# Kernel optimization log

Measured on AMD Instinct MI355X. Metric: run time of the kernel, lower is better.

Reference implementation:

```python
import jax, jax.numpy as jnp
import numpy as np

K = 8                      # batch_k
NONZERO_CUTOFF = 1.4       # nonzero_loss_cutoff
MARGIN = 1.0               # F.triplet_margin_loss default (module's margin arg is unused)
PD_EPS = 1e-6              # torch pairwise_distance eps


def setup_inputs() -> dict:
    key = jax.random.key(0)
    x = jax.random.normal(key, (4096, 128), dtype=jnp.float32)
    return {"x": x}


def _sample_indices(x, key):
    """Distance-weighted negative sampling; returns (a_idx, p_idx, n_idx), each [n*(K-1)]."""
    n, d = x.shape
    # per-row L2 normalize (eps added to norm, as in original)
    xn = x / (jnp.sqrt(jnp.sum(x * x, axis=1, keepdims=True)) + 1e-5)
    # pairwise euclidean distance; identity added under sqrt exactly as original
    sq = jnp.sum(xn * xn, axis=1, keepdims=True)               # [n,1]
    dist2 = sq + sq.T - 2.0 * (xn @ xn.T)                       # [n,n]
    dist = jnp.sqrt(dist2 + jnp.eye(n, dtype=x.dtype))          # [n,n]
    # distance-weighted sampling log-weights (Wu et al.)
    log_w = (2.0 - d) * jnp.log(dist) - (d - 3) / 2.0 * jnp.log(1.0 - 0.25 * dist * dist)
    w = jnp.exp(log_w - jnp.max(log_w))
    # block mask: same-block pairs excluded
    block = jnp.arange(n) // K                                  # [n]
    mask = (block[:, None] != block[None, :]).astype(x.dtype)
    w = w * mask * (dist < NONZERO_CUTOFF).astype(x.dtype)
    row_sum = jnp.sum(w, axis=1, keepdims=True)
    # rows where weights are degenerate fall back to uniform (original's try/except)
    valid = jnp.isfinite(row_sum) & (row_sum > 0) & jnp.all(jnp.isfinite(w), axis=1, keepdims=True)
    logits = jnp.where(valid, jnp.where(w > 0, jnp.log(w), -jnp.inf), 0.0)   # [n,n]
    # batched categorical sampling via Gumbel-max: K-1 negatives per anchor
    g = jax.random.gumbel(key, (n, K - 1, n), dtype=jnp.float32)
    n_idx = jnp.argmax(logits[:, None, :] + g, axis=-1).reshape(-1)          # [n*(K-1)]
    # anchor/positive pairs: for each i, all other members of its block
    r = jnp.arange(n) % K                                       # position in block
    off = jnp.arange(K - 1)
    p_off = jnp.where(off[None, :] < r[:, None], off[None, :], off[None, :] + 1)
    p_idx = (block[:, None] * K + p_off).reshape(-1)            # [n*(K-1)]
    a_idx = jnp.repeat(jnp.arange(n), K - 1)                    # [n*(K-1)]
    return a_idx, p_idx, n_idx


def reference(x) -> jnp.ndarray:
    key = jax.random.key(42)
    a_idx, p_idx, n_idx = _sample_indices(x, key)
    a, p, ng = x[a_idx], x[p_idx], x[n_idx]
    d_ap = jnp.sqrt(jnp.sum((a - p + PD_EPS) ** 2, axis=1))
    d_an = jnp.sqrt(jnp.sum((a - ng + PD_EPS) ** 2, axis=1))
    return jnp.mean(jnp.maximum(d_ap - d_an + MARGIN, 0.0))
```

## Files before the change

kernel.cpp:

```cpp
#include <hip/hip_runtime.h>
#include <stdint.h>

#define NROWS 4096
#define DIM   128
#define KB    8
#define NS    7
#define TCH   16
#define NPAIR 2048
#define HALF_CNT 58720256u

typedef __bf16 v8bf __attribute__((ext_vector_type(8)));
typedef float  v4f  __attribute__((ext_vector_type(4)));

__device__ __forceinline__ uint32_t rotl32(uint32_t x, int r) {
    return __builtin_amdgcn_alignbit(x, x, 32 - r);
}

__device__ __forceinline__ void threefry2x32(uint32_t c0, uint32_t c1,
                                             uint32_t& o0, uint32_t& o1) {
    const uint32_t ks0 = 0u;
    const uint32_t ks1 = 42u;
    const uint32_t ks2 = 0x1BD11BDAu ^ ks0 ^ ks1;
    uint32_t x0 = c0 + ks0;
    uint32_t x1 = c1 + ks1;
#define TF_R(r) { x0 += x1; x1 = rotl32(x1, r); x1 ^= x0; }
    TF_R(13) TF_R(15) TF_R(26) TF_R(6)
    x0 += ks1; x1 += ks2 + 1u;
    TF_R(17) TF_R(29) TF_R(16) TF_R(24)
    x0 += ks2; x1 += ks0 + 2u;
    TF_R(13) TF_R(15) TF_R(26) TF_R(6)
    x0 += ks0; x1 += ks1 + 3u;
    TF_R(17) TF_R(29) TF_R(16) TF_R(24)
    x0 += ks1; x1 += ks2 + 4u;
    TF_R(13) TF_R(15) TF_R(26) TF_R(6)
    x0 += ks2; x1 += ks0 + 5u;
#undef TF_R
    o0 = x0; o1 = x1;
}

__device__ __forceinline__ float gumbel_of(uint32_t b) {
    float f = __uint_as_float((b >> 9) | 0x3f800000u) - 1.0f;
    float u = f + 1.17549435e-38f;
    float l1 = __log2f(u);
    float inner = -0.69314718055994531f * l1;
    float l2 = __log2f(inner);
    return -0.69314718055994531f * l2;
}

__global__ void knorm(const float* __restrict__ x, __bf16* __restrict__ xb,
                      float* __restrict__ sqv) {
    const int i = blockIdx.x;
    const int t = threadIdx.x;
    float2 v = ((const float2*)(x + (size_t)i * DIM))[t];
    float s = v.x * v.x + v.y * v.y;
#pragma unroll
    for (int m = 32; m > 0; m >>= 1) s += __shfl_xor(s, m, 64);
    float norm = sqrtf(s) + 1e-5f;
    float ox = v.x / norm, oy = v.y / norm;
    union { __bf16 b[2]; uint32_t u; } ph;
    ph.b[0] = (__bf16)ox; ph.b[1] = (__bf16)oy;
    ((uint32_t*)xb)[i * 64 + t] = ph.u;
    float s2 = ox * ox + oy * oy;
#pragma unroll
    for (int m = 32; m > 0; m >>= 1) s2 += __shfl_xor(s2, m, 64);
    if (t == 0) sqv[i] = s2;
}

__global__ __launch_bounds__(256, 4) void kdist(
        const __bf16* __restrict__ xb, const float* __restrict__ sqv,
        int* __restrict__ cnt, unsigned short* __restrict__ t16,
        float2* __restrict__ nwp) {
    const int lane  = threadIdx.x & 63;
    const int chunk = (blockIdx.x << 2) + (threadIdx.x >> 6);
    const int grp   = blockIdx.y;
    const int rlo = lane & 15;
    const int khi = lane >> 4;
    const unsigned int below = (1u << rlo) - 1u;

    const int afr = grp * 8 + (rlo >> 1) + ((rlo & 1) << 11);
    v8bf ah[4];
#pragma unroll
    for (int ks = 0; ks < 4; ++ks)
        ah[ks] = *(const v8bf*)(xb + (size_t)afr * DIM + ks * 32 + khi * 8);

    const int base = grp * 8 + khi * 2;
    float sqA[4];
    sqA[0] = sqv[base];
    sqA[1] = sqv[base + 2048];
    sqA[2] = sqv[base + 1];
    sqA[3] = sqv[base + 2049];

    const int rbA = ((base)     * 16 + chunk) << 8;
    const int rbB = ((base + 1) * 16 + chunk) << 8;
    unsigned int cA = 0, cB = 0;

    const int tcol0 = chunk * 256 + rlo;

    v8bf bhn[4];
    float sqn;
    {
        const size_t boff = (size_t)tcol0 * DIM + khi * 8;
#pragma unroll
        for (int ks = 0; ks < 4; ++ks) bhn[ks] = *(const v8bf*)(xb + boff + ks * 32);
        sqn = sqv[tcol0];
    }

#pragma unroll 1
    for (int cg = 0; cg < 16; ++cg) {
        v8bf bhc[4];
#pragma unroll
        for (int ks = 0; ks < 4; ++ks) bhc[ks] = bhn[ks];
        const float sqB = sqn;
        const int tcol = tcol0 + cg * 16;

        if (cg < 15) {
            const size_t boff = (size_t)(tcol + 16) * DIM + khi * 8;
#pragma unroll
            for (int ks = 0; ks < 4; ++ks) bhn[ks] = *(const v8bf*)(xb + boff + ks * 32);
            sqn = sqv[tcol + 16];
        }

        v4f acc = {0.f, 0.f, 0.f, 0.f};
#pragma unroll
        for (int ks = 0; ks < 4; ++ks)
            acc = __builtin_amdgcn_mfma_f32_16x16x32_bf16(ah[ks], bhc[ks], acc, 0, 0, 0);

        const int tBlk = tcol >> 3;
        const bool bd0 = (tBlk != grp);
        const bool bd1 = (tBlk != grp + 256);

        float nw[4];
        bool  ic[4];
#pragma unroll
        for (int q = 0; q < 4; ++q) {
            float d2  = fmaf(-2.0f, acc[q], sqA[q] + sqB);
            float l1  = __log2f(d2);
            float t2  = fmaf(-0.25f, d2, 1.0f);
            float l2  = __log2f(t2);
            float wiv = exp2f(fmaf(63.0f, l1, 62.5f * l2));
            bool incl = (d2 < 1.96f) && ((q & 1) ? bd1 : bd0);
            ic[q] = incl;
            nw[q] = incl ? -wiv : -INFINITY;
        }

        const bool uA = ic[0] | ic[1];
        const bool uB = ic[2] | ic[3];
        unsigned long long ballA = __ballot(uA);
        unsigned long long ballB = __ballot(uB);
        unsigned int subA = (unsigned int)((ballA >> (khi * 16)) & 0xFFFFull);
        unsigned int subB = (unsigned int)((ballB >> (khi * 16)) & 0xFFFFull);
        if (uA) {
            int slot = rbA + (int)cA + __popc(subA & below);
            t16[slot] = (unsigned short)tcol;
            nwp[slot] = make_float2(nw[0], nw[1]);
        }
        if (uB) {
            int slot = rbB + (int)cB + __popc(subB & below);
            t16[slot] = (unsigned short)tcol;
            nwp[slot] = make_float2(nw[2], nw[3]);
        }
        cA += (unsigned int)__popc(subA);
        cB += (unsigned int)__popc(subB);
    }

    if (rlo == 0) {
        cnt[base * 16 + chunk]       = (int)cA;
        cnt[(base + 1) * 16 + chunk] = (int)cB;
    }
}

__global__ __launch_bounds__(256, 4) void kgum(
        const int* __restrict__ cnt, const unsigned short* __restrict__ t16,
        const float2* __restrict__ nwp, int* __restrict__ nidx) {
    const int p    = blockIdx.x;
    const int wid  = threadIdx.x >> 6;
    const int lane = threadIdx.x & 63;
    const uint32_t pb0 = ((uint32_t)p * 7u) << 12;

    unsigned long long bA[NS], bB[NS];
#pragma unroll
    for (int j = 0; j < NS; ++j) { bA[j] = ~0ull; bB[j] = ~0ull; }

#pragma unroll 1
    for (int c = wid * 4; c < wid * 4 + 4; ++c) {
        const int rid = p * 16 + c;
        const int n  = cnt[rid];
        const int rb = rid << 8;
#pragma unroll 1
        for (int e = lane; e < n; e += 64) {
            const uint32_t t = t16[rb + e];
            const float2 nw  = nwp[rb + e];
#pragma unroll
            for (int j = 0; j < NS; ++j) {
                const uint32_t L = pb0 + ((uint32_t)j << 12) + t;
                uint32_t o0, o1;
                threefry2x32(L, L + HALF_CNT, o0, o1);
                float fA = __uint_as_float((o0 >> 9) | 0x3f800000u) - 1.0f;
                float fB = __uint_as_float((o1 >> 9) | 0x3f800000u) - 1.0f;
                float kA = __log2f(fA + 1.17549435e-38f) * nw.x;
                float kB = __log2f(fB + 1.17549435e-38f) * nw.y;
                unsigned long long pA =
                    ((unsigned long long)__float_as_uint(kA) << 32) | t;
                unsigned long long pB =
                    ((unsigned long long)__float_as_uint(kB) << 32) | t;
                bA[j] = pA < bA[j] ? pA : bA[j];
                bB[j] = pB < bB[j] ? pB : bB[j];
            }
        }
    }

#pragma unroll
    for (int j = 0; j < NS; ++j) {
#pragma unroll
        for (int m = 1; m < 64; m <<= 1) {
            unsigned long long vA = __shfl_xor(bA[j], m, 64);
            unsigned long long vB = __shfl_xor(bB[j], m, 64);
            bA[j] = vA < bA[j] ? vA : bA[j];
            bB[j] = vB < bB[j] ? vB : bB[j];
        }
    }

    __shared__ unsigned long long sA[4][NS], sB[4][NS];
    if (lane == 0) {
#pragma unroll
        for (int j = 0; j < NS; ++j) { sA[wid][j] = bA[j]; sB[wid][j] = bB[j]; }
    }
    __syncthreads();
    if (threadIdx.x < 2 * NS) {
        const int r = threadIdx.x / NS, j = threadIdx.x - r * NS;
        unsigned long long v = r ? sB[0][j] : sA[0][j];
#pragma unroll
        for (int w = 1; w < 4; ++w) {
            unsigned long long v2 = r ? sB[w][j] : sA[w][j];
            v = v2 < v ? v2 : v;
        }
        uint32_t kb = (uint32_t)(v >> 32);
        nidx[(p + r * 2048) * NS + j] = (kb >= 0x7F800000u) ? -1
                                                            : (int)(v & 0xFFFFu);
    }
}

__global__ __launch_bounds__(256, 2) void ksample(
        const __bf16* __restrict__ xb, const float* __restrict__ sqv,
        float* __restrict__ pV, int* __restrict__ pI) {
    const int lane  = threadIdx.x & 63;
    const int chunk = (blockIdx.x << 2) + (threadIdx.x >> 6);
    const int grp   = blockIdx.y;
    const int rlo = lane & 15;
    const int khi = lane >> 4;

    const int afr = grp * 8 + (rlo >> 1) + ((rlo & 1) << 11);
    v8bf ah[4];
#pragma unroll
    for (int ks = 0; ks < 4; ++ks)
        ah[ks] = *(const v8bf*)(xb + (size_t)afr * DIM + ks * 32 + khi * 8);
    const int base = grp * 8 + khi * 2;
    float sqA[4];
    sqA[0] = sqv[base];
    sqA[1] = sqv[base + 2048];
    sqA[2] = sqv[base + 1];
    sqA[3] = sqv[base + 2049];
    const uint32_t P0 = (uint32_t)base;
    const uint32_t P1 = (uint32_t)(base + 1);

    float    bestV[4][NS];
    uint32_t bestP[4];
#pragma unroll
    for (int q = 0; q < 4; ++q) {
        bestP[q] = 0u;
#pragma unroll
        for (int j = 0; j < NS; ++j) bestV[q][j] = INFINITY;
    }
    const int tcol0 = chunk * 256 + rlo;

    v8bf bhn[4];
    float sqn;
    {
        const size_t boff = (size_t)tcol0 * DIM + khi * 8;
#pragma unroll
        for (int ks = 0; ks < 4; ++ks) bhn[ks] = *(const v8bf*)(xb + boff + ks * 32);
        sqn = sqv[tcol0];
    }

#pragma unroll 1
    for (int cg = 0; cg < 16; ++cg) {
        v8bf bhc[4];
#pragma unroll
        for (int ks = 0; ks < 4; ++ks) bhc[ks] = bhn[ks];
        const float sqB = sqn;
        const int tcol = tcol0 + cg * 16;
        if (cg < 15) {
            const size_t boff = (size_t)(tcol + 16) * DIM + khi * 8;
#pragma unroll
            for (int ks = 0; ks < 4; ++ks) bhn[ks] = *(const v8bf*)(xb + boff + ks * 32);
            sqn = sqv[tcol + 16];
        }
        v4f acc = {0.f, 0.f, 0.f, 0.f};
#pragma unroll
        for (int ks = 0; ks < 4; ++ks)
            acc = __builtin_amdgcn_mfma_f32_16x16x32_bf16(ah[ks], bhc[ks], acc, 0, 0, 0);
        const int tBlk = tcol >> 3;
        const bool bd0 = (tBlk != grp);
        const bool bd1 = (tBlk != grp + 256);
        float nw[4];
#pragma unroll
        for (int q = 0; q < 4; ++q) {
            float d2  = fmaf(-2.0f, acc[q], sqA[q] + sqB);
            float l1  = __log2f(d2);
            float t2  = fmaf(-0.25f, d2, 1.0f);
            float l2  = __log2f(t2);
            float wiv = exp2f(fmaf(63.0f, l1, 62.5f * l2));
            bool incl = (d2 < 1.96f) && ((q & 1) ? bd1 : bd0);
            nw[q] = incl ? -wiv : -INFINITY;
        }
        const uint32_t tB = (uint32_t)tcol;
#pragma unroll
        for (int j = 0; j < NS; ++j) {
            uint32_t L0 = ((P0 * 7u + (uint32_t)j) << 12) + tB;
            uint32_t L1 = ((P1 * 7u + (uint32_t)j) << 12) + tB;
            uint32_t o0, o1, o2, o3;
            threefry2x32(L0, L0 + HALF_CNT, o0, o1);
            threefry2x32(L1, L1 + HALF_CNT, o2, o3);
            float vv[4];
            vv[0] = __log2f(__uint_as_float((o0 >> 9) | 0x3f800000u) - 1.0f + 1.17549435e-38f) * nw[0];
            vv[1] = __log2f(__uint_as_float((o1 >> 9) | 0x3f800000u) - 1.0f + 1.17549435e-38f) * nw[1];
            vv[2] = __log2f(__uint_as_float((o2 >> 9) | 0x3f800000u) - 1.0f + 1.17549435e-38f) * nw[2];
            vv[3] = __log2f(__uint_as_float((o3 >> 9) | 0x3f800000u) - 1.0f + 1.17549435e-38f) * nw[3];
            const uint32_t keep = ~(0xFu << (4 * j));
            const uint32_t put  = ((uint32_t)cg) << (4 * j);
#pragma unroll
            for (int q = 0; q < 4; ++q) {
                bool lt = vv[q] < bestV[q][j];
                uint32_t np = (bestP[q] & keep) | put;
                bestV[q][j] = lt ? vv[q] : bestV[q][j];
                bestP[q]    = lt ? np : bestP[q];
            }
        }
    }
#pragma unroll
    for (int q = 0; q < 4; ++q) {
        const int a = base + (q >> 1) + ((q & 1) << 11);
#pragma unroll
        for (int j = 0; j < NS; ++j) {
            float v = bestV[q][j];
            int idx = tcol0 + (int)((bestP[q] >> (4 * j)) & 0xFu) * 16;
#pragma unroll
            for (int m = 1; m < 16; m <<= 1) {
                float v2 = __shfl_xor(v, m, 16);
                int   i2 = __shfl_xor(idx, m, 16);
                if (v2 < v || (v2 == v && i2 < idx)) { v = v2; idx = i2; }
            }
            if (rlo == 0) {
                size_t s = ((size_t)a * NS + j) * TCH + chunk;
                pV[s] = v;
                pI[s] = idx;
            }
        }
    }
}

__global__ void kcombine(const float* __restrict__ pV, const int* __restrict__ pI,
                         int* __restrict__ nidx, int nc) {
    int s = blockIdx.x * 256 + threadIdx.x;
    if (s >= NROWS * NS) return;
    float bv = INFINITY;
    int bi = 0x7FFFFFFF;
    for (int c = 0; c < nc; ++c) {
        float v = pV[(size_t)s * nc + c];
        int idx = pI[(size_t)s * nc + c];
        if (v < bv || (v == bv && idx < bi)) { bv = v; bi = idx; }
    }
    nidx[s] = (bv == INFINITY) ? -1 : bi;
}

__global__ void kfixup(int* __restrict__ nidx) {
    const int i = blockIdx.x;
    if (nidx[(size_t)i * NS] >= 0) return;
    const int lane = threadIdx.x;
    for (int j = 0; j < NS; ++j) {
        float bv = -INFINITY;
        int bi = 0x7FFFFFFF;
        for (int t = lane; t < NROWS; t += 64) {
            uint32_t o0, o1;
            float g;
            if (i < 2048) {
                uint32_t L = (((uint32_t)(i * NS + j)) << 12) + (uint32_t)t;
                threefry2x32(L, L + HALF_CNT, o0, o1);
                g = gumbel_of(o0);
            } else {
                uint32_t L = (((uint32_t)((i - 2048) * NS + j)) << 12) + (uint32_t)t;
                threefry2x32(L, L + HALF_CNT, o0, o1);
                g = gumbel_of(o1);
            }
            if (g > bv) { bv = g; bi = t; }
        }
#pragma unroll
        for (int m = 1; m < 64; m <<= 1) {
            float v2 = __shfl_xor(bv, m, 64);
            int   i2 = __shfl_xor(bi, m, 64);
            if (v2 > bv || (v2 == bv && i2 < bi)) { bv = v2; bi = i2; }
        }
        if (lane == 0) nidx[i * NS + j] = bi;
    }
}

__global__ void kloss(const float* __restrict__ x, const int* __restrict__ nidx,
                      float* __restrict__ loss) {
    int s = blockIdx.x * 256 + threadIdx.x;
    if (s >= NROWS * NS) return;
    int i = s / NS, j = s - i * NS;
    int r = i & (KB - 1), blk = i >> 3;
    int po = (j < r) ? j : j + 1;
    int p = blk * KB + po;
    int n = nidx[s] & (NROWS - 1);
    const float4* A  = (const float4*)(x + (size_t)i * DIM);
    const float4* P  = (const float4*)(x + (size_t)p * DIM);
    const float4* Ng = (const float4*)(x + (size_t)n * DIM);
    float sap = 0.0f, san = 0.0f;
#pragma unroll 8
    for (int k = 0; k < DIM / 4; ++k) {
        float4 a = A[k], pv = P[k], nv = Ng[k];
        float d;
        d = a.x - pv.x + 1e-6f; sap += d * d;
        d = a.y - pv.y + 1e-6f; sap += d * d;
        d = a.z - pv.z + 1e-6f; sap += d * d;
        d = a.w - pv.w + 1e-6f; sap += d * d;
        d = a.x - nv.x + 1e-6f; san += d * d;
        d = a.y - nv.y + 1e-6f; san += d * d;
        d = a.z - nv.z + 1e-6f; san += d * d;
        d = a.w - nv.w + 1e-6f; san += d * d;
    }
    loss[s] = fmaxf(sqrtf(sap) - sqrtf(san) + 1.0f, 0.0f);
}

__global__ void kreduce(const float* __restrict__ loss, float* __restrict__ out) {
    __shared__ float part[4];
    const int tid = threadIdx.x;
    float sum = 0.0f;
    for (int s = tid; s < NROWS * NS; s += 256) sum += loss[s];
#pragma unroll
    for (int m = 32; m > 0; m >>= 1) sum += __shfl_xor(sum, m, 64);
    if ((tid & 63) == 0) part[tid >> 6] = sum;
    __syncthreads();
    if (tid == 0) out[0] = (part[0] + part[1] + part[2] + part[3]) / 28672.0f;
}

extern "C" void kernel_launch(void* const* d_in, const int* in_sizes, int n_in,
                              void* d_out, int out_size, void* d_ws, size_t ws_size,
                              hipStream_t stream) {
    const float* x = (const float*)d_in[0];
    float* out = (float*)d_out;

    uint8_t* w = (uint8_t*)d_ws;
    size_t off = 0;
    auto take = [&](size_t bytes) {
        void* p = w + off;
        off = (off + bytes + 255) & ~(size_t)255;
        return p;
    };
    __bf16* xb   = (__bf16*)take((size_t)NROWS * DIM * 2);
    float*  sqv  = (float*)take((size_t)NROWS * 4);
    int*    nidx = (int*)take((size_t)NROWS * NS * 4);
    float*  loss = (float*)take((size_t)NROWS * NS * 4);
    int*    cnt  = (int*)take((size_t)NPAIR * 16 * 4);
    const size_t prefix = off;
    const size_t t16_b = (size_t)NPAIR * 16 * 256 * 2;
    const size_t nwp_b = (size_t)NPAIR * 16 * 256 * 8;
    const size_t NEED_BIG = prefix + ((t16_b + 255) & ~(size_t)255)
                          + ((nwp_b + 255) & ~(size_t)255);

    knorm<<<NROWS, 64, 0, stream>>>(x, xb, sqv);

    if (ws_size >= NEED_BIG) {
        unsigned short* t16 = (unsigned short*)take(t16_b);
        float2*         nwp = (float2*)take(nwp_b);
        kdist<<<dim3(TCH / 4, 256), 256, 0, stream>>>(xb, sqv, cnt, t16, nwp);
        kgum<<<NPAIR, 256, 0, stream>>>(cnt, t16, nwp, nidx);
    } else {
        float* pV = (float*)take((size_t)NROWS * NS * TCH * 4);
        int*   pI = (int*)take((size_t)NROWS * NS * TCH * 4);
        ksample<<<dim3(TCH / 4, 256), 256, 0, stream>>>(xb, sqv, pV, pI);
        kcombine<<<(NROWS * NS + 255) / 256, 256, 0, stream>>>(pV, pI, nidx, TCH);
    }

    kfixup<<<NROWS, 64, 0, stream>>>(nidx);
    kloss<<<(NROWS * NS + 255) / 256, 256, 0, stream>>>(x, nidx, loss);
    kreduce<<<1, 256, 0, stream>>>(loss, out);
}
```

Baseline: 189.3 us.

## Split Gumbel argmax across two blocks per pair, merge with 64-bit atomicMin

The Gumbel-max kernel now launches two blocks per row pair, each covering half of the 16 candidate chunks, and each wave flattens its two chunks into a single lane-strided loop so lanes stay balanced across uneven chunk counts. Partial argmin results are merged through 64-bit atomicMin into a packed buffer that is memset to all ones beforehand. A new small kernel then unpacks the index. The aim is more parallelism and less per-wave tail imbalance, at the cost of an extra memset, an extra launch and global atomics.

```diff
diff --git a/kernel.cpp b/kernel.cpp
--- a/kernel.cpp
+++ b/kernel.cpp
@@ -171,41 +171,46 @@
 
 __global__ __launch_bounds__(256, 4) void kgum(
         const int* __restrict__ cnt, const unsigned short* __restrict__ t16,
-        const float2* __restrict__ nwp, int* __restrict__ nidx) {
-    const int p    = blockIdx.x;
+        const float2* __restrict__ nwp, unsigned long long* __restrict__ pk) {
+    const int bid  = blockIdx.x;
+    const int p    = bid >> 1;
+    const int half = bid & 1;
     const int wid  = threadIdx.x >> 6;
     const int lane = threadIdx.x & 63;
     const uint32_t pb0 = ((uint32_t)p * 7u) << 12;
 
+    const int rid0 = p * 16 + half * 8 + wid * 2;
+    const int n0 = cnt[rid0];
+    const int n1 = cnt[rid0 + 1];
+    const int tot = n0 + n1;
+    const int rb0 = rid0 << 8;
+
     unsigned long long bA[NS], bB[NS];
 #pragma unroll
     for (int j = 0; j < NS; ++j) { bA[j] = ~0ull; bB[j] = ~0ull; }
 
 #pragma unroll 1
-    for (int c = wid * 4; c < wid * 4 + 4; ++c) {
-        const int rid = p * 16 + c;
-        const int n  = cnt[rid];
-        const int rb = rid << 8;
-#pragma unroll 1
-        for (int e = lane; e < n; e += 64) {
-            const uint32_t t = t16[rb + e];
-            const float2 nw  = nwp[rb + e];
-#pragma unroll
-            for (int j = 0; j < NS; ++j) {
-                const uint32_t L = pb0 + ((uint32_t)j << 12) + t;
-                uint32_t o0, o1;
-                threefry2x32(L, L + HALF_CNT, o0, o1);
-                float fA = __uint_as_float((o0 >> 9) | 0x3f800000u) - 1.0f;
-                float fB = __uint_as_float((o1 >> 9) | 0x3f800000u) - 1.0f;
-                float kA = __log2f(fA + 1.17549435e-38f) * nw.x;
-                float kB = __log2f(fB + 1.17549435e-38f) * nw.y;
-                unsigned long long pA =
-                    ((unsigned long long)__float_as_uint(kA) << 32) | t;
-                unsigned long long pB =
-                    ((unsigned long long)__float_as_uint(kB) << 32) | t;
-                bA[j] = pA < bA[j] ? pA : bA[j];
-                bB[j] = pB < bB[j] ? pB : bB[j];
-            }
+    for (int g = lane; g < tot; g += 64) {
+        const int r = (g >= n0) ? 1 : 0;
+        const int off = r ? (g - n0) : g;
+        const int idx = rb0 + (r << 8) + off;
+        const uint32_t t = t16[idx];
+        const float2 nw  = nwp[idx];
+#pragma unroll
+        for (int j = 0; j < NS; ++j) {
+            const uint32_t L = pb0 + ((uint32_t)j << 12) + t;
+            uint32_t o0, o1;
+            threefry2x32(L, L + HALF_CNT, o0, o1);
+            float fA = __uint_as_float((o0 >> 9) | 0x3f800000u) - 1.0f;
+            float fB = __uint_as_float((o1 >> 9) | 0x3f800000u) - 1.0f;
+            float kA = __log2f(fA + 1.17549435e-38f) * nw.x;
+            float kB = __log2f(fB + 1.17549435e-38f) * nw.y;
+            unsigned long long pA =
+                ((unsigned long long)__float_as_uint(kA) << 32) | t;
+            unsigned long long pB =
+                ((unsigned long long)__float_as_uint(kB) << 32) | t;
+            bA[j] = pA < bA[j] ? pA : bA[j];
+            bB[j] = pB < bB[j] ? pB : bB[j];
         }
     }
 
@@ -234,10 +239,17 @@
             unsigned long long v2 = r ? sB[w][j] : sA[w][j];
             v = v2 < v ? v2 : v;
         }
-        uint32_t kb = (uint32_t)(v >> 32);
-        nidx[(p + r * 2048) * NS + j] = (kb >= 0x7F800000u) ? -1
-                                                            : (int)(v & 0xFFFFu);
-    }
+        atomicMin(&pk[(size_t)(p + r * 2048) * NS + j], v);
+    }
+}
+
+__global__ void kextract(const unsigned long long* __restrict__ pk,
+                         int* __restrict__ nidx) {
+    int s = blockIdx.x * 256 + threadIdx.x;
+    if (s >= NROWS * NS) return;
+    unsigned long long v = pk[s];
+    uint32_t kb = (uint32_t)(v >> 32);
+    nidx[s] = (kb >= 0x7F800000u) ? -1 : (int)(v & 0xFFFFu);
 }
 
 __global__ __launch_bounds__(256, 2) void ksample(
@@ -463,6 +475,7 @@
     int*    nidx = (int*)take((size_t)NROWS * NS * 4);
     float*  loss = (float*)take((size_t)NROWS * NS * 4);
     int*    cnt  = (int*)take((size_t)NPAIR * 16 * 4);
+    unsigned long long* pk = (unsigned long long*)take((size_t)NROWS * NS * 8);
     const size_t prefix = off;
     const size_t t16_b = (size_t)NPAIR * 16 * 256 * 2;
     const size_t nwp_b = (size_t)NPAIR * 16 * 256 * 8;
@@ -474,8 +487,10 @@
     if (ws_size >= NEED_BIG) {
         unsigned short* t16 = (unsigned short*)take(t16_b);
         float2*         nwp = (float2*)take(nwp_b);
+        hipMemsetAsync(pk, 0xFF, (size_t)NROWS * NS * 8, stream);
         kdist<<<dim3(TCH / 4, 256), 256, 0, stream>>>(xb, sqv, cnt, t16, nwp);
-        kgum<<<NPAIR, 256, 0, stream>>>(cnt, t16, nwp, nidx);
+        kgum<<<NPAIR * 2, 256, 0, stream>>>(cnt, t16, nwp, pk);
+        kextract<<<(NROWS * NS + 255) / 256, 256, 0, stream>>>(pk, nidx);
     } else {
         float* pV = (float*)take((size_t)NROWS * NS * TCH * 4);
         int*   pI = (int*)take((size_t)NROWS * NS * TCH * 4);
```

New measurement: 193.9 us. +2.4%, slower.
